# Kernel optimization log

Hardware: AMD Instinct MI355X
Metric: run time of the kernel (lower is better)

## Reference

```python
import jax, jax.numpy as jnp
import numpy as np

B, S, D, H = 4, 2048, 512, 8
HD = D // H


def _xavier(key, shape):
    fan_in, fan_out = shape[1], shape[0]
    limit = float(np.sqrt(6.0 / (fan_in + fan_out)))
    return jax.random.uniform(key, shape, jnp.float32, -limit, limit)


def setup_inputs() -> dict:
    key = jax.random.key(0)
    ks = jax.random.split(key, 7)
    return {
        "query": jax.random.normal(ks[0], (B, S, D), jnp.float32),
        "key": jax.random.normal(ks[1], (B, S, D), jnp.float32),
        "value": jax.random.normal(ks[2], (B, S, D), jnp.float32),
        "Wq": _xavier(ks[3], (D, D)), "bq": jnp.zeros((D,), jnp.float32),
        "Wk": _xavier(ks[4], (D, D)), "bk": jnp.zeros((D,), jnp.float32),
        "Wv": _xavier(ks[5], (D, D)), "bv": jnp.zeros((D,), jnp.float32),
        "Wo": _xavier(ks[6], (D, D)), "bo": jnp.zeros((D,), jnp.float32),
    }


def _split_heads(x):
    # [B,S,D] -> [B,H,S,HD]
    return x.reshape(B, S, H, HD).transpose(0, 2, 1, 3)


def reference(query, key, value, Wq, bq, Wk, bk, Wv, bv, Wo, bo):
    # torch Linear: y = x @ W.T + b
    Q = _split_heads(query @ Wq.T + bq)
    K = _split_heads(key @ Wk.T + bk)
    V = _split_heads(value @ Wv.T + bv)
    scale = 1.0 / jnp.sqrt(jnp.asarray(HD, Q.dtype))
    logits = jnp.einsum("bhqd,bhkd->bhqk", Q, K) * scale  # [B,H,S,S]
    attn = jax.nn.softmax(logits, axis=-1)
    ctx = jnp.einsum("bhqk,bhkd->bhqd", attn, V)
    ctx = ctx.transpose(0, 2, 1, 3).reshape(B, S, D)
    return ctx @ Wo.T + bo
```

## Files before the change

### kernel.cpp

```cpp
#include <hip/hip_runtime.h>
#include <hip/hip_bf16.h>


#define BB 4
#define SS 2048
#define DD 512
#define HH 8
#define HDD 64

typedef __bf16 bf16;
typedef __bf16 bf16x8 __attribute__((ext_vector_type(8)));
typedef float f32x4 __attribute__((ext_vector_type(4)));
typedef float f32x16 __attribute__((ext_vector_type(16)));

__device__ __forceinline__ int swz(int row, int byteInRow) {
    return row * 128 + (byteInRow ^ ((row & 7) << 4));
}

__device__ __forceinline__ void gload16(const void* g, void* l) {
    __builtin_amdgcn_global_load_lds(
        (const __attribute__((address_space(1))) void*)g,
        (__attribute__((address_space(3))) void*)l, 16, 0, 0);
}

__global__ __launch_bounds__(256) void cvt_bf16(
    const float* __restrict__ xq, const float* __restrict__ xk, const float* __restrict__ xv,
    const float* __restrict__ wq, const float* __restrict__ wk, const float* __restrict__ wv,
    const float* __restrict__ wo,
    bf16* __restrict__ xqb, bf16* __restrict__ xkb, bf16* __restrict__ xvb,
    bf16* __restrict__ wqb, bf16* __restrict__ wkb, bf16* __restrict__ wvb,
    bf16* __restrict__ wob)
{
    const int NX = BB * SS * DD / 4;
    const int NW = DD * DD / 4;
    const int total = 3 * NX + 4 * NW;
    for (int g = blockIdx.x * 256 + threadIdx.x; g < total; g += gridDim.x * 256) {
        const float* src; bf16* dst; int off;
        if (g < 3 * NX) {
            int s = g >> 20; off = g & (NX - 1);
            src = s == 0 ? xq : s == 1 ? xk : xv;
            dst = s == 0 ? xqb : s == 1 ? xkb : xvb;
        } else {
            int gg = g - 3 * NX; int s = gg >> 16; off = gg & (NW - 1);
            src = s == 0 ? wq : s == 1 ? wk : s == 2 ? wv : wo;
            dst = s == 0 ? wqb : s == 1 ? wkb : s == 2 ? wvb : wob;
        }
        float4 v = ((const float4*)src)[off];
        union { bf16 h[4]; ushort4 u; } c;
        c.h[0] = (bf16)v.x; c.h[1] = (bf16)v.y; c.h[2] = (bf16)v.z; c.h[3] = (bf16)v.w;
        ((ushort4*)dst)[off] = c.u;
    }
}

__global__ __launch_bounds__(256) void gemm_qkv(
    const bf16* __restrict__ Xq, const bf16* __restrict__ Xk, const bf16* __restrict__ Xv,
    const bf16* __restrict__ Wq, const bf16* __restrict__ Wk, const bf16* __restrict__ Wv,
    const float* __restrict__ bq, const float* __restrict__ bk, const float* __restrict__ bv,
    bf16* __restrict__ Qb, bf16* __restrict__ Kb, bf16* __restrict__ Vt)
{
    const int lin = blockIdx.x;
    const int w = (lin & 7) * 96 + (lin >> 3);
    const int z = w >> 8, rem = w & 255;
    const int m0 = (rem >> 2) * 128, n0 = (rem & 3) * 128;

    const bf16* __restrict__ A  = (z == 0) ? Xq : (z == 1) ? Xk : Xv;
    const bf16* __restrict__ Wt = (z == 0) ? Wq : (z == 1) ? Wk : Wv;
    const float* __restrict__ bias = (z == 0) ? bq : (z == 1) ? bk : bv;

    __shared__ char lds[32768];
    char* As = lds;
    char* Bs = lds + 16384;

    const int t = threadIdx.x, wid = t >> 6, lane = t & 63;
    const int wr = wid >> 1, wc = wid & 1;
    const int lr = lane & 15, lg = lane >> 4;

    float bv4[4];
#pragma unroll
    for (int ni = 0; ni < 4; ni++) bv4[ni] = bias[n0 + wc * 64 + ni * 16 + lr];

    const int srow = lane >> 3, s_l = (lane & 7) ^ srow;

    f32x4 acc[4][4] = {};

    for (int k0 = 0; k0 < DD; k0 += 64) {
#pragma unroll
        for (int i = 0; i < 4; i++) {
            int row = 32 * wid + 8 * i + srow;
            gload16(A  + (size_t)(m0 + row) * DD + k0 + s_l * 8, As + (32 * wid + 8 * i) * 128);
            gload16(Wt + (size_t)(n0 + row) * DD + k0 + s_l * 8, Bs + (32 * wid + 8 * i) * 128);
        }
        __syncthreads();
#pragma unroll
        for (int kk = 0; kk < 2; kk++) {
            bf16x8 af[4], bfr[4];
#pragma unroll
            for (int mi = 0; mi < 4; mi++)
                af[mi] = *(const bf16x8*)(As + swz(wr * 64 + mi * 16 + lr, kk * 64 + lg * 16));
#pragma unroll
            for (int ni = 0; ni < 4; ni++)
                bfr[ni] = *(const bf16x8*)(Bs + swz(wc * 64 + ni * 16 + lr, kk * 64 + lg * 16));
#pragma unroll
            for (int mi = 0; mi < 4; mi++)
#pragma unroll
                for (int ni = 0; ni < 4; ni++)
                    acc[mi][ni] = __builtin_amdgcn_mfma_f32_16x16x32_bf16(af[mi], bfr[ni], acc[mi][ni], 0, 0, 0);
        }
        __syncthreads();
    }

#pragma unroll
    for (int mi = 0; mi < 4; mi++)
#pragma unroll
        for (int ni = 0; ni < 4; ni++) {
            int col = n0 + wc * 64 + ni * 16 + lr;
#pragma unroll
            for (int j = 0; j < 4; j++) {
                int row = m0 + wr * 64 + mi * 16 + lg * 4 + j;
                float v = acc[mi][ni][j] + bv4[ni];
                if (z == 0) {
                    Qb[(size_t)row * DD + col] = (bf16)v;
                } else if (z == 1) {
                    Kb[(size_t)row * DD + col] = (bf16)v;
                } else {
                    int b = row >> 11, s = row & 2047, h = col >> 6, d = col & 63;
                    Vt[((((size_t)b * HH + h) * HDD + d) << 11) + s] = (bf16)v;
                }
            }
        }
}

__global__ __launch_bounds__(256) void attn_kernel(
    const bf16* __restrict__ Qb, const bf16* __restrict__ Kb,
    const bf16* __restrict__ Vt, bf16* __restrict__ Ctx)
{
    __shared__ char lds[32768];
    const int t = threadIdx.x, wid = t >> 6, lane = t & 63;
    const int l31 = lane & 31, hi = lane >> 5;
    const int lin = blockIdx.x;
    const int wk = (lin & 7) * 64 + (lin >> 3);
    const int qt = wk & 15, bh = wk >> 4;
    const int b = bh >> 3, h = bh & 7;
    const int q0 = qt * 128 + wid * 32;

    const bf16* Qp = Qb + ((size_t)b * SS + q0) * DD + h * HDD;
    const bf16* Kp = Kb + (size_t)b * SS * DD + h * HDD;
    const bf16* Vp = Vt + ((size_t)b * HH + h) * HDD * SS;

    const float qscale = 0.125f * 1.4426950408889634f;
    bf16x8 qf[4];
#pragma unroll
    for (int dk = 0; dk < 4; dk++) {
        bf16x8 v = *(const bf16x8*)(Qp + (size_t)l31 * DD + dk * 16 + hi * 8);
#pragma unroll
        for (int e = 0; e < 8; e++) v[e] = (bf16)((float)v[e] * qscale);
        qf[dk] = v;
    }

    bf16x8 ones;
#pragma unroll
    for (int e = 0; e < 8; e++) ones[e] = (bf16)1.0f;

    const int srow = lane >> 3, s_l = (lane & 7) ^ srow;
    const size_t koff = (size_t)(16 * wid + srow) * DD + s_l * 8;
    const size_t voff = (size_t)(16 * wid + srow) * SS + s_l * 8;

#define STAGE(buf, kvb) do {                                                   \
        char* Kd = lds + (buf) * 8192 + wid * 2048;                            \
        char* Vd = lds + 16384 + (buf) * 8192 + wid * 2048;                    \
        gload16(Kp + koff + (size_t)(kvb) * DD, Kd);                           \
        gload16(Kp + koff + 8 * DD + (size_t)(kvb) * DD, Kd + 1024);           \
        gload16(Vp + voff + (kvb), Vd);                                        \
        gload16(Vp + voff + 8 * SS + (kvb), Vd + 1024);                        \
    } while (0)

    STAGE(0, 0);

    f32x16 ctx0 = {}, ctx1 = {}, l4 = {};
    __syncthreads();

    const int NT = SS / 64;
    for (int it = 0; it < NT; ++it) {
        const int cur = it & 1;
        const char* Ks = lds + cur * 8192;
        const char* Vs = lds + 16384 + cur * 8192;
        if (it + 1 < NT) STAGE(cur ^ 1, (it + 1) * 64);

        f32x16 p0 = {}, p1 = {};
        __builtin_amdgcn_s_setprio(1);
#pragma unroll
        for (int dk = 0; dk < 4; dk++) {
            bf16x8 kf0 = *(const bf16x8*)(Ks + swz(l31,      dk * 32 + hi * 16));
            bf16x8 kf1 = *(const bf16x8*)(Ks + swz(32 + l31, dk * 32 + hi * 16));
            p0 = __builtin_amdgcn_mfma_f32_32x32x16_bf16(kf0, qf[dk], p0, 0, 0, 0);
            p1 = __builtin_amdgcn_mfma_f32_32x32x16_bf16(kf1, qf[dk], p1, 0, 0, 0);
        }
        __builtin_amdgcn_s_setprio(0);

#pragma unroll
        for (int r = 0; r < 16; r++) {
            p0[r] = __builtin_amdgcn_exp2f(p0[r]);
            p1[r] = __builtin_amdgcn_exp2f(p1[r]);
        }

#define PVBLOCK(P, NTOFF) do {                                                       \
        union { bf16 h[8]; bf16x8 v; } F0, F1;                                       \
        _Pragma("unroll")                                                            \
        for (int e = 0; e < 8; e++) { F0.h[e] = (bf16)P[e]; F1.h[e] = (bf16)P[8 + e]; } \
        l4 = __builtin_amdgcn_mfma_f32_32x32x16_bf16(F0.v, ones, l4, 0, 0, 0);       \
        l4 = __builtin_amdgcn_mfma_f32_32x32x16_bf16(F1.v, ones, l4, 0, 0, 0);       \
        union { ushort4 q[2]; bf16x8 v; } v00, v01, v10, v11;                        \
        v00.q[0] = *(const ushort4*)(Vs + swz(l31,      (NTOFF) + 8 * hi));          \
        v00.q[1] = *(const ushort4*)(Vs + swz(l31,      (NTOFF) + 16 + 8 * hi));     \
        v01.q[0] = *(const ushort4*)(Vs + swz(32 + l31, (NTOFF) + 8 * hi));          \
        v01.q[1] = *(const ushort4*)(Vs + swz(32 + l31, (NTOFF) + 16 + 8 * hi));     \
        v10.q[0] = *(const ushort4*)(Vs + swz(l31,      (NTOFF) + 32 + 8 * hi));     \
        v10.q[1] = *(const ushort4*)(Vs + swz(l31,      (NTOFF) + 48 + 8 * hi));     \
        v11.q[0] = *(const ushort4*)(Vs + swz(32 + l31, (NTOFF) + 32 + 8 * hi));     \
        v11.q[1] = *(const ushort4*)(Vs + swz(32 + l31, (NTOFF) + 48 + 8 * hi));     \
        ctx0 = __builtin_amdgcn_mfma_f32_32x32x16_bf16(F0.v, v00.v, ctx0, 0, 0, 0);  \
        ctx0 = __builtin_amdgcn_mfma_f32_32x32x16_bf16(F1.v, v10.v, ctx0, 0, 0, 0);  \
        ctx1 = __builtin_amdgcn_mfma_f32_32x32x16_bf16(F0.v, v01.v, ctx1, 0, 0, 0);  \
        ctx1 = __builtin_amdgcn_mfma_f32_32x32x16_bf16(F1.v, v11.v, ctx1, 0, 0, 0);  \
    } while (0)

        PVBLOCK(p0, 0);
        PVBLOCK(p1, 64);
#undef PVBLOCK
        __syncthreads();
    }
#undef STAGE

#pragma unroll
    for (int r = 0; r < 16; r++) {
        int q = (r & 3) + 8 * (r >> 2) + 4 * hi;
        float inv = 1.0f / l4[r];
        size_t base = ((size_t)b * SS + q0 + q) * DD + h * HDD;
        Ctx[base + l31]      = (bf16)(ctx0[r] * inv);
        Ctx[base + 32 + l31] = (bf16)(ctx1[r] * inv);
    }
}

__global__ __launch_bounds__(256) void gemm_out(
    const bf16* __restrict__ A, const bf16* __restrict__ Wt,
    const float* __restrict__ bias, float* __restrict__ Out)
{
    const int lin = blockIdx.x;
    const int w = (lin & 7) * 32 + (lin >> 3);
    const int m0 = (w >> 2) * 128, n0 = (w & 3) * 128;

    __shared__ char lds[32768];
    char* As = lds;
    char* Bs = lds + 16384;

    const int t = threadIdx.x, wid = t >> 6, lane = t & 63;
    const int wr = wid >> 1, wc = wid & 1;
    const int lr = lane & 15, lg = lane >> 4;

    float bv4[4];
#pragma unroll
    for (int ni = 0; ni < 4; ni++) bv4[ni] = bias[n0 + wc * 64 + ni * 16 + lr];

    const int srow = lane >> 3, s_l = (lane & 7) ^ srow;

    f32x4 acc[4][4] = {};

    for (int k0 = 0; k0 < DD; k0 += 64) {
#pragma unroll
        for (int i = 0; i < 4; i++) {
            int row = 32 * wid + 8 * i + srow;
            gload16(A  + (size_t)(m0 + row) * DD + k0 + s_l * 8, As + (32 * wid + 8 * i) * 128);
            gload16(Wt + (size_t)(n0 + row) * DD + k0 + s_l * 8, Bs + (32 * wid + 8 * i) * 128);
        }
        __syncthreads();
#pragma unroll
        for (int kk = 0; kk < 2; kk++) {
            bf16x8 af[4], bfr[4];
#pragma unroll
            for (int mi = 0; mi < 4; mi++)
                af[mi] = *(const bf16x8*)(As + swz(wr * 64 + mi * 16 + lr, kk * 64 + lg * 16));
#pragma unroll
            for (int ni = 0; ni < 4; ni++)
                bfr[ni] = *(const bf16x8*)(Bs + swz(wc * 64 + ni * 16 + lr, kk * 64 + lg * 16));
#pragma unroll
            for (int mi = 0; mi < 4; mi++)
#pragma unroll
                for (int ni = 0; ni < 4; ni++)
                    acc[mi][ni] = __builtin_amdgcn_mfma_f32_16x16x32_bf16(af[mi], bfr[ni], acc[mi][ni], 0, 0, 0);
        }
        __syncthreads();
    }

#pragma unroll
    for (int mi = 0; mi < 4; mi++)
#pragma unroll
        for (int ni = 0; ni < 4; ni++) {
            int col = n0 + wc * 64 + ni * 16 + lr;
#pragma unroll
            for (int j = 0; j < 4; j++) {
                int row = m0 + wr * 64 + mi * 16 + lg * 4 + j;
                Out[(size_t)row * DD + col] = acc[mi][ni][j] + bv4[ni];
            }
        }
}

extern "C" void kernel_launch(void* const* d_in, const int* in_sizes, int n_in,
                              void* d_out, int out_size, void* d_ws, size_t ws_size,
                              hipStream_t stream) {
    (void)in_sizes; (void)n_in; (void)out_size; (void)ws_size;
    const float* q  = (const float*)d_in[0];
    const float* k  = (const float*)d_in[1];
    const float* v  = (const float*)d_in[2];
    const float* Wq = (const float*)d_in[3]; const float* bq = (const float*)d_in[4];
    const float* Wk = (const float*)d_in[5]; const float* bk = (const float*)d_in[6];
    const float* Wv = (const float*)d_in[7]; const float* bv = (const float*)d_in[8];
    const float* Wo = (const float*)d_in[9]; const float* bo = (const float*)d_in[10];
    float* out = (float*)d_out;

    char* ws = (char*)d_ws;
    const size_t MD2 = (size_t)BB * SS * DD * 2;
    const size_t WB  = (size_t)DD * DD * 2;
    bf16* Qb  = (bf16*)(ws);
    bf16* Kb  = (bf16*)(ws + MD2);
    bf16* Vt  = (bf16*)(ws + 2 * MD2);
    bf16* Ctx = (bf16*)(ws + 3 * MD2);
    bf16* Xqb = Ctx;
    bf16* Xkb = (bf16*)(ws + 4 * MD2);
    bf16* Xvb = (bf16*)(ws + 5 * MD2);
    bf16* Wqb = (bf16*)(ws + 6 * MD2);
    bf16* Wkb = (bf16*)(ws + 6 * MD2 + WB);
    bf16* Wvb = (bf16*)(ws + 6 * MD2 + 2 * WB);
    bf16* Wob = (bf16*)(ws + 6 * MD2 + 3 * WB);

    cvt_bf16<<<2048, 256, 0, stream>>>(q, k, v, Wq, Wk, Wv, Wo,
                                       Xqb, Xkb, Xvb, Wqb, Wkb, Wvb, Wob);

    gemm_qkv<<<768, 256, 0, stream>>>(Xqb, Xkb, Xvb, Wqb, Wkb, Wvb,
                                      bq, bk, bv, Qb, Kb, Vt);

    attn_kernel<<<512, 256, 0, stream>>>(Qb, Kb, Vt, Ctx);

    gemm_out<<<256, 256, 0, stream>>>(Ctx, Wob, bo, out);
}
```

Measured before the change: 127.5 us.

## Split KV sequence across two wave groups per attention block with LDS reduction

The attention block grows to 512 threads organised as two groups of four waves. Each group handles alternating 64-key tiles of the sequence for the same 128 queries, so each wave runs half as many iterations. At the end the second group writes its partial context and row sums into LDS, and the first group adds them and writes the normalised output. This raises wave count per block and per CU to hide latency, at the cost of doubling LDS use, an extra barrier and a reduction step.

```diff
diff --git a/kernel.cpp b/kernel.cpp
--- a/kernel.cpp
+++ b/kernel.cpp
@@ -130,18 +130,19 @@
         }
 }
 
-__global__ __launch_bounds__(256) void attn_kernel(
+__global__ __launch_bounds__(512) void attn_kernel(
     const bf16* __restrict__ Qb, const bf16* __restrict__ Kb,
     const bf16* __restrict__ Vt, bf16* __restrict__ Ctx)
 {
-    __shared__ char lds[32768];
+    __shared__ char lds[65536];
     const int t = threadIdx.x, wid = t >> 6, lane = t & 63;
+    const int grp = wid >> 2, qw = wid & 3;
     const int l31 = lane & 31, hi = lane >> 5;
     const int lin = blockIdx.x;
     const int wk = (lin & 7) * 64 + (lin >> 3);
     const int qt = wk & 15, bh = wk >> 4;
     const int b = bh >> 3, h = bh & 7;
-    const int q0 = qt * 128 + wid * 32;
+    const int q0 = qt * 128 + qw * 32;
 
     const bf16* Qp = Qb + ((size_t)b * SS + q0) * DD + h * HDD;
     const bf16* Kp = Kb + (size_t)b * SS * DD + h * HDD;
@@ -162,29 +163,29 @@
     for (int e = 0; e < 8; e++) ones[e] = (bf16)1.0f;
 
     const int srow = lane >> 3, s_l = (lane & 7) ^ srow;
-    const size_t koff = (size_t)(16 * wid + srow) * DD + s_l * 8;
-    const size_t voff = (size_t)(16 * wid + srow) * SS + s_l * 8;
+    const size_t koff = (size_t)(16 * qw + srow) * DD + s_l * 8;
+    const size_t voff = (size_t)(16 * qw + srow) * SS + s_l * 8;
 
 #define STAGE(buf, kvb) do {                                                   \
-        char* Kd = lds + (buf) * 8192 + wid * 2048;                            \
-        char* Vd = lds + 16384 + (buf) * 8192 + wid * 2048;                    \
+        char* Kd = lds + grp * 16384 + (buf) * 8192 + qw * 2048;               \
+        char* Vd = lds + 32768 + grp * 16384 + (buf) * 8192 + qw * 2048;       \
         gload16(Kp + koff + (size_t)(kvb) * DD, Kd);                           \
         gload16(Kp + koff + 8 * DD + (size_t)(kvb) * DD, Kd + 1024);           \
         gload16(Vp + voff + (kvb), Vd);                                        \
         gload16(Vp + voff + 8 * SS + (kvb), Vd + 1024);                        \
     } while (0)
 
-    STAGE(0, 0);
+    STAGE(0, grp * 64);
 
     f32x16 ctx0 = {}, ctx1 = {}, l4 = {};
     __syncthreads();
 
-    const int NT = SS / 64;
-    for (int it = 0; it < NT; ++it) {
+    const int NI = SS / 128;
+    for (int it = 0; it < NI; ++it) {
         const int cur = it & 1;
-        const char* Ks = lds + cur * 8192;
-        const char* Vs = lds + 16384 + cur * 8192;
-        if (it + 1 < NT) STAGE(cur ^ 1, (it + 1) * 64);
+        const char* Ks = lds + grp * 16384 + cur * 8192;
+        const char* Vs = lds + 32768 + grp * 16384 + cur * 8192;
+        if (it + 1 < NI) STAGE(cur ^ 1, (it + 1) * 128 + grp * 64);
 
         f32x16 p0 = {}, p1 = {};
         __builtin_amdgcn_s_setprio(1);
@@ -231,13 +232,32 @@
     }
 #undef STAGE
 
-#pragma unroll
-    for (int r = 0; r < 16; r++) {
-        int q = (r & 3) + 8 * (r >> 2) + 4 * hi;
-        float inv = 1.0f / l4[r];
-        size_t base = ((size_t)b * SS + q0 + q) * DD + h * HDD;
-        Ctx[base + l31]      = (bf16)(ctx0[r] * inv);
-        Ctx[base + 32 + l31] = (bf16)(ctx1[r] * inv);
+    if (grp == 1) {
+        float* dst = (float*)(lds + qw * 12288);
+#pragma unroll
+        for (int r = 0; r < 16; r++) {
+            dst[r * 64 + lane]        = ctx0[r];
+            dst[(16 + r) * 64 + lane] = ctx1[r];
+            dst[(32 + r) * 64 + lane] = l4[r];
+        }
+    }
+    __syncthreads();
+    if (grp == 0) {
+        const float* src = (const float*)(lds + qw * 12288);
+#pragma unroll
+        for (int r = 0; r < 16; r++) {
+            ctx0[r] += src[r * 64 + lane];
+            ctx1[r] += src[(16 + r) * 64 + lane];
+            l4[r]   += src[(32 + r) * 64 + lane];
+        }
+#pragma unroll
+        for (int r = 0; r < 16; r++) {
+            int q = (r & 3) + 8 * (r >> 2) + 4 * hi;
+            float inv = 1.0f / l4[r];
+            size_t base = ((size_t)b * SS + q0 + q) * DD + h * HDD;
+            Ctx[base + l31]      = (bf16)(ctx0[r] * inv);
+            Ctx[base + 32 + l31] = (bf16)(ctx1[r] * inv);
+        }
     }
 }
 
@@ -338,7 +358,7 @@
     gemm_qkv<<<768, 256, 0, stream>>>(Xqb, Xkb, Xvb, Wqb, Wkb, Wvb,
                                       bq, bk, bv, Qb, Kb, Vt);
 
-    attn_kernel<<<512, 256, 0, stream>>>(Qb, Kb, Vt, Ctx);
+    attn_kernel<<<512, 512, 0, stream>>>(Qb, Kb, Vt, Ctx);
 
     gemm_out<<<256, 256, 0, stream>>>(Ctx, Wob, bo, out);
 }
```

After: 121.4 us. 1.05x faster.
